# Kernel tuning notes

Measured on AMD Instinct MI355X. Metric: run time of the kernel, lower is better.

## Reference

```python
import jax, jax.numpy as jnp
import numpy as np

# --- fake-quant helpers (Brevitas-style simulated int4 with STE) ---

def _fq(x, scale, qmin, qmax):
    # fake quantize with straight-through estimator
    q = jnp.clip(jnp.round(x / scale), qmin, qmax) * scale
    return x + jax.lax.stop_gradient(q - x)

def quant_act_signed4(x):
    # signed 4-bit symmetric activation quant: scale = max|x| / 7
    scale = jax.lax.stop_gradient(jnp.maximum(jnp.max(jnp.abs(x)), 1e-8) / 7.0)
    return _fq(x, scale, -8, 7), scale

def quant_relu4(x):
    # QuantReLU: relu then unsigned 4-bit quant, scale = max / 15
    x = jax.nn.relu(x)
    scale = jax.lax.stop_gradient(jnp.maximum(jnp.max(x), 1e-8) / 15.0)
    return _fq(x, scale, 0, 15), scale

def quant_w4(w):
    # per-tensor symmetric 4-bit weight quant
    scale = jax.lax.stop_gradient(jnp.maximum(jnp.max(jnp.abs(w)), 1e-8) / 7.0)
    return _fq(w, scale, -8, 7), scale

def quant_bias32(b, in_scale, w_scale):
    # Int32Bias: bias quantized at scale = input_scale * weight_scale
    s = in_scale * w_scale
    return _fq(b, s, -(2.0**31), 2.0**31 - 1.0)

def conv2d(x, w, b):
    y = jax.lax.conv_general_dilated(x, w, (1, 1), 'VALID',
                                     dimension_numbers=('NCHW', 'OIHW', 'NCHW'))
    return y + b[None, :, None, None]


def setup_inputs() -> dict:
    key = jax.random.key(0)
    ks = jax.random.split(key, 9)
    f32 = jnp.float32
    return {
        'x':   jax.random.normal(ks[0], (32, 3, 224, 224), f32),
        'w1':  jax.random.normal(ks[1], (32, 3, 3, 3), f32) * 0.1,
        'b1':  jax.random.normal(ks[2], (32,), f32) * 0.05,
        'w2':  jax.random.normal(ks[3], (64, 32, 3, 3), f32) * 0.06,
        'b2':  jax.random.normal(ks[4], (64,), f32) * 0.05,
        'wf1': jax.random.normal(ks[5], (128, 64), f32) * 0.1,
        'bf1': jax.random.normal(ks[6], (128,), f32) * 0.05,
        'wf2': jax.random.normal(ks[7], (10, 128), f32) * 0.08,
        'bf2': jax.random.normal(ks[8], (10,), f32) * 0.05,
    }


def reference(x, w1, b1, w2, b2, wf1, bf1, wf2, bf2):
    # quant_inp
    xq, s_in = quant_act_signed4(x)
    # conv1 (quantized weights, Int32 bias)
    w1q, sw1 = quant_w4(w1)
    y = conv2d(xq, w1q, quant_bias32(b1, s_in, sw1))
    y, s1 = quant_relu4(y)
    # conv2
    w2q, sw2 = quant_w4(w2)
    y = conv2d(y, w2q, quant_bias32(b2, s1, sw2))
    y, s2 = quant_relu4(y)
    # adaptive avg pool to 1x1 + flatten -> [B, 64]
    y = jnp.mean(y, axis=(2, 3))
    # fc1
    wf1q, swf1 = quant_w4(wf1)
    y = y @ wf1q.T + quant_bias32(bf1, s2, swf1)
    y, s3 = quant_relu4(y)
    # fc2
    wf2q, swf2 = quant_w4(wf2)
    y = y @ wf2q.T + quant_bias32(bf2, s3, swf2)
    return jax.nn.log_softmax(y, axis=1)
```

## Files before the change

kernel.cpp:

```cpp
#include <hip/hip_runtime.h>
#include <cstdint>
#include <cstddef>

#define DI __device__ __forceinline__

typedef int v4i  __attribute__((ext_vector_type(4)));
typedef int v16i __attribute__((ext_vector_type(16)));

#if defined(__has_builtin)
#if __has_builtin(__builtin_amdgcn_sdot4)
#define HAS_SDOT4 1
#endif
#if __has_builtin(__builtin_amdgcn_alignbyte)
#define HAS_ALIGNBYTE 1
#endif
#if __has_builtin(__builtin_amdgcn_global_load_lds)
#define HAS_GLLDS 1
#endif
#if __has_builtin(__builtin_amdgcn_perm)
#define HAS_PERM 1
#endif
#endif

DI int dot4(unsigned a, unsigned b, int c) {
#ifdef HAS_SDOT4
  return __builtin_amdgcn_sdot4((int)a, (int)b, c, false);
#else
#pragma unroll
  for (int k = 0; k < 4; ++k)
    c += (int)(signed char)(a >> (8 * k)) * (int)(signed char)(b >> (8 * k));
  return c;
#endif
}

DI unsigned alignb(unsigned hi, unsigned lo, int sh) {
#ifdef HAS_ALIGNBYTE
  return __builtin_amdgcn_alignbyte(hi, lo, sh);
#else
  return sh ? ((lo >> (8 * sh)) | (hi << (32 - 8 * sh))) : lo;
#endif
}

DI unsigned bperm(unsigned hi, unsigned lo, unsigned sel) {
#ifdef HAS_PERM
  return __builtin_amdgcn_perm(hi, lo, sel);
#else
  unsigned r = 0;
#pragma unroll
  for (int i = 0; i < 4; ++i) {
    unsigned s = (sel >> (8 * i)) & 255u;
    unsigned b = (s < 4) ? (lo >> (8 * s)) : (hi >> (8 * (s - 4)));
    r |= (b & 255u) << (8 * i);
  }
  return r;
#endif
}

DI float qclamp(int a, float h) {
  return fminf(fmaxf(rintf((float)a * h), 0.f), 15.f);
}

DI unsigned pack4(float4 v, float s) {
  float f[4] = {v.x, v.y, v.z, v.w};
  unsigned w = 0;
#pragma unroll
  for (int k = 0; k < 4; ++k) {
    float q = rintf(f[k] / s);
    q = fminf(fmaxf(q, -8.f), 7.f);
    w |= ((unsigned)((int)q & 255)) << (8 * k);
  }
  return w;
}

#ifdef HAS_GLLDS
typedef __attribute__((address_space(1))) void glb_void;
typedef __attribute__((address_space(3))) void lds_void;
DI void gl_lds16(const void* g, void* l) {
  __builtin_amdgcn_global_load_lds((const glb_void*)g, (lds_void*)l, 16, 0, 0);
}
#else
DI void gl_lds16(const void* g, void* l) { *(v4i*)l = *(const v4i*)g; }
#endif

struct Scal {
  unsigned max_x, max_w1, max_w2, max_wf1, max_wf2;
  int max1, max2;
};

DI float mkscale(unsigned bits, float d) { return fmaxf(__uint_as_float(bits), 1e-8f) / d; }
DI float d_s_in(const Scal* sc) { return mkscale(sc->max_x, 7.f); }
DI float d_sw1(const Scal* sc)  { return mkscale(sc->max_w1, 7.f); }
DI float d_sw2(const Scal* sc)  { return mkscale(sc->max_w2, 7.f); }
DI float d_s1(const Scal* sc)   { return fmaxf((float)sc->max1 * (d_s_in(sc) * d_sw1(sc)), 1e-8f) / 15.f; }
DI float d_s2(const Scal* sc)   { return fmaxf((float)sc->max2 * (d_s1(sc) * d_sw2(sc)), 1e-8f) / 15.f; }

static constexpr int NX   = 32 * 3 * 224 * 224;
static constexpr int NP1  = 32 * 32 * 222 * 224;
static constexpr int C2_ROWB   = 224 * 32;
static constexpr int C2_HPLANE = 224 * 16;
static constexpr int C2_GRID = 32 * 110;

DI float wave_maxf(float v) { for (int o = 32; o; o >>= 1) v = fmaxf(v, __shfl_down(v, o, 64)); return v; }
DI int   wave_maxi(int v)   { for (int o = 32; o; o >>= 1) v = max(v, __shfl_down(v, o, 64));   return v; }

DI float block_maxf(float v) {
  __shared__ float s[8];
  v = wave_maxf(v);
  int lane = threadIdx.x & 63, w = threadIdx.x >> 6;
  int nw = (int)(blockDim.x >> 6);
  if (!lane) s[w] = v;
  __syncthreads();
  if (threadIdx.x < 64) {
    float t = ((int)threadIdx.x < nw) ? s[threadIdx.x] : 0.f;
    v = wave_maxf(t);
  }
  return v;
}

DI int block_maxi(int v) {
  __shared__ int s[8];
  v = wave_maxi(v);
  int lane = threadIdx.x & 63, w = threadIdx.x >> 6;
  int nw = (int)(blockDim.x >> 6);
  if (!lane) s[w] = v;
  __syncthreads();
  if (threadIdx.x < 64) {
    int t = ((int)threadIdx.x < nw) ? s[threadIdx.x] : 0;
    v = wave_maxi(t);
  }
  return v;
}

__global__ void k_absmax_xw(const float4* __restrict__ x, int n4,
                            const float* __restrict__ w1, const float* __restrict__ w2,
                            const float* __restrict__ wf1, const float* __restrict__ wf2,
                            Scal* sc) {
  if (blockIdx.x < 1024) {
    float m = 0.f;
    for (int i = blockIdx.x * 256 + threadIdx.x; i < n4; i += 1024 * 256) {
      float4 v = x[i];
      m = fmaxf(m, fmaxf(fmaxf(fabsf(v.x), fabsf(v.y)), fmaxf(fabsf(v.z), fabsf(v.w))));
    }
    m = block_maxf(m);
    if (!threadIdx.x) atomicMax(&sc->max_x, __float_as_uint(m));
    return;
  }
  const float* p; int n; unsigned* slot;
  int wb = blockIdx.x - 1024;
  if (wb == 0)      { p = w1;  n = 864;   slot = &sc->max_w1; }
  else if (wb == 1) { p = w2;  n = 18432; slot = &sc->max_w2; }
  else if (wb == 2) { p = wf1; n = 8192;  slot = &sc->max_wf1; }
  else              { p = wf2; n = 1280;  slot = &sc->max_wf2; }
  float m = 0.f;
  for (int i = threadIdx.x; i < n; i += 256) m = fmaxf(m, fabsf(p[i]));
  m = block_maxf(m);
  if (!threadIdx.x) atomicMax(slot, __float_as_uint(m));
}


DI void kpack0(const unsigned* R, v4i& f) {
  f[0] = (int)bperm(R[1], R[0], 0x04020100u);
  f[1] = (int)bperm(R[2], R[1], 0x05040201u);
  f[2] = (int)bperm(R[3], R[2], 0x06050402u);
  f[3] = (int)bperm(R[5], R[4], 0x04020100u);
}
DI void kpack1(const unsigned* R, v4i& f) {
  f[0] = (int)bperm(R[1], R[0], 0x05040201u);
  f[1] = (int)bperm(R[2], R[1], 0x06050402u);
  f[2] = (int)bperm(0u,   R[3], 0x04020100u);
  f[3] = 0;
}

DI v4i conv1_afrag(const unsigned* lw, int oc, int lhalf) {
  unsigned R[6];
  v4i f;
  if (lhalf == 0) {
#pragma unroll
    for (int s = 0; s < 6; ++s) R[s] = lw[oc * 9 + s];
    kpack0(R, f);
  } else {
#pragma unroll
    for (int s = 0; s < 4; ++s) R[s] = lw[oc * 9 + 5 + s];
    kpack1(R, f);
  }
  return f;
}

DI v4i conv1_bfrag(const signed char* lx, int oh_l, int qb, int sh, int lhalf) {
  unsigned R[6];
  v4i f;
  if (lhalf == 0) {
#pragma unroll
    for (int s = 0; s < 6; ++s) {
      int ic = s / 3, kh = s - ic * 3;
      const signed char* base = lx + (ic * 8 + oh_l + kh) * 224 + qb;
      unsigned d0 = *(const unsigned*)base;
      unsigned d1 = *(const unsigned*)(base + 4);
      R[s] = alignb(d1, d0, sh);
    }
    kpack0(R, f);
  } else {
#pragma unroll
    for (int s = 0; s < 4; ++s) {
      int seg = 5 + s;
      int ic = seg / 3, kh = seg - ic * 3;
      const signed char* base = lx + (ic * 8 + oh_l + kh) * 224 + qb;
      unsigned d0 = *(const unsigned*)base;
      unsigned d1 = *(const unsigned*)(base + 4);
      R[s] = alignb(d1, d0, sh);
    }
    kpack1(R, f);
  }
  return f;
}

DI void conv1_stage(const float4* x, const float* w1, const float* b1,
                    int b, int oh0, int tid, float s_in, float sw1,
                    signed char* lx, unsigned* lw, int* lb) {
  for (int i = tid; i < 288; i += 448) {
    int oc = i / 9, r = i - oc * 9;
    unsigned w = 0;
#pragma unroll
    for (int k = 0; k < 3; ++k) {
      float q = rintf(w1[oc * 27 + r * 3 + k] / sw1);
      q = fminf(fmaxf(q, -8.f), 7.f);
      w |= ((unsigned)((int)q & 255)) << (8 * k);
    }
    lw[i] = w;
  }
  if (tid < 32) lb[tid] = (int)rintf(b1[tid] / (s_in * sw1));
  const float4* src = x + (size_t)b * 3 * 224 * 56;
  unsigned* dst = (unsigned*)lx;
#pragma unroll
  for (int it = 0; it < 3; ++it) {
    int i = it * 448 + tid;
    int row = i / 56, d = i - row * 56;
    int ic = row >> 3, r = row & 7;
    dst[i] = pack4(src[(ic * 224 + (oh0 + r)) * 56 + d], s_in);
  }
}

__global__ void __launch_bounds__(448) k_conv1a(
    const float4* __restrict__ x, const float* __restrict__ w1,
    const float* __restrict__ b1, const float* __restrict__ w2,
    const Scal* __restrict__ sc, unsigned* __restrict__ w2frag,
    int* __restrict__ max1) {
  int tid = threadIdx.x;
  if (blockIdx.x >= 1184) {
    int j = (blockIdx.x - 1184) * 448 + tid;
    if (j < 4608) {
      int icq = j & 7; int t = j >> 3;
      int kw = t % 3; t /= 3;
      int kh = t % 3; int oc = t / 3;
      float s = d_sw2(sc);
      unsigned w = 0;
#pragma unroll
      for (int k = 0; k < 4; ++k) {
        int ic = icq * 4 + k;
        float q = rintf(w2[(oc * 32 + ic) * 9 + kh * 3 + kw] / s);
        q = fminf(fmaxf(q, -8.f), 7.f);
        w |= ((unsigned)((int)q & 255)) << (8 * k);
      }
      int tap = kh * 3 + kw;
      int dl = (oc & 31) | ((icq >> 2) << 5);
      w2frag[(((tap * 2) + (oc >> 5)) * 64 + dl) * 4 + (icq & 3)] = w;
    }
    return;
  }

  __shared__ signed char lx[3 * 8 * 224 + 16];
  __shared__ unsigned lw[288];
  __shared__ int lb[32];
  int strip = blockIdx.x % 37;
  int b = blockIdx.x / 37;
  int oh0 = strip * 6;
  float s_in = d_s_in(sc), sw1 = d_sw1(sc);
  conv1_stage(x, w1, b1, b, oh0, tid, s_in, sw1, lx, lw, lb);
  __syncthreads();

  int lane = tid & 63, wv = tid >> 6;
  int lane31 = lane & 31, lhalf = lane >> 5;
  int p = wv * 32 + lane31;
  int qb = p & ~3, sh = p & 3;
  v4i af = conv1_afrag(lw, lane31, lhalf);
  const v4i* lbv = (const v4i*)lb;
  v4i bq[4];
#pragma unroll
  for (int q = 0; q < 4; ++q) bq[q] = lbv[lhalf + 2 * q];

  int mx = 0;
#pragma unroll
  for (int oh_l = 0; oh_l < 6; ++oh_l) {
    v4i bf = conv1_bfrag(lx, oh_l, qb, sh, lhalf);
    v16i acc;
#pragma unroll
    for (int q = 0; q < 4; ++q)
#pragma unroll
      for (int j = 0; j < 4; ++j) acc[4 * q + j] = bq[q][j];
    acc = __builtin_amdgcn_mfma_i32_32x32x32_i8(af, bf, acc, 0, 0, 0);
    if (p < 222) {
#pragma unroll
      for (int r = 0; r < 16; ++r) mx = max(mx, acc[r]);
    }
  }
  mx = block_maxi(max(mx, 0));
  if (!tid) atomicMax(max1, mx);
}

__global__ void __launch_bounds__(448) k_conv1b(
    const float4* __restrict__ x, const float* __restrict__ w1,
    const float* __restrict__ b1, const Scal* __restrict__ sc,
    unsigned char* __restrict__ y1n) {
  __shared__ signed char lx[3 * 8 * 224 + 16];
  __shared__ unsigned lw[288];
  __shared__ int lb[32];
  int tid = threadIdx.x;
  int strip = blockIdx.x % 37;
  int b = blockIdx.x / 37;
  int oh0 = strip * 6;
  float s_in = d_s_in(sc), sw1 = d_sw1(sc);
  conv1_stage(x, w1, b1, b, oh0, tid, s_in, sw1, lx, lw, lb);
  __syncthreads();

  int lane = tid & 63, wv = tid >> 6;
  int lane31 = lane & 31, lhalf = lane >> 5;
  int p = wv * 32 + lane31;
  int qb = p & ~3, sh = p & 3;
  v4i af = conv1_afrag(lw, lane31, lhalf);
  const v4i* lbv = (const v4i*)lb;
  v4i bq[4];
#pragma unroll
  for (int q = 0; q < 4; ++q) bq[q] = lbv[lhalf + 2 * q];

  float h1 = (s_in * sw1) / d_s1(sc);

#pragma unroll
  for (int oh_l = 0; oh_l < 6; ++oh_l) {
    v4i bf = conv1_bfrag(lx, oh_l, qb, sh, lhalf);
    v16i acc;
#pragma unroll
    for (int q = 0; q < 4; ++q)
#pragma unroll
      for (int j = 0; j < 4; ++j) acc[4 * q + j] = bq[q][j];
    acc = __builtin_amdgcn_mfma_i32_32x32x32_i8(af, bf, acc, 0, 0, 0);
    if (p < 222) {
      size_t rowb = (size_t)(b * 222 + oh0 + oh_l) * C2_ROWB;
      unsigned char* dst0 = y1n + rowb + (size_t)p * 16;
#pragma unroll
      for (int q = 0; q < 4; ++q) {
        int oc0 = 8 * q + 4 * lhalf;
        unsigned cw = 0;
#pragma unroll
        for (int j = 0; j < 4; ++j)
          cw |= ((unsigned)(int)qclamp(acc[4 * q + j], h1)) << (8 * j);
        *(unsigned*)(dst0 + (oc0 >> 4) * C2_HPLANE + (oc0 & 15)) = cw;
      }
    }
  }
}


DI void c2_stage(const unsigned char* gA, const unsigned char* gW,
                 unsigned char* lA, unsigned* lw, int tid) {
  for (int c = tid; c < 2944; c += 448) {
    if (c < 1792) gl_lds16(gA + (size_t)c * 16, lA + c * 16);
    else          gl_lds16(gW + (size_t)(c - 1792) * 16,
                           (unsigned char*)lw + (size_t)(c - 1792) * 16);
  }
}

__global__ void __launch_bounds__(448, 4) k_conv2a(
    const unsigned char* __restrict__ y1n, const unsigned* __restrict__ w2frag,
    const float* __restrict__ b2, const Scal* __restrict__ sc, int* __restrict__ max2) {
  __shared__ __align__(16) unsigned char lA[4 * C2_ROWB];
  __shared__ __align__(16) unsigned lw[4608];
  __shared__ int lb2[64];
  int tid = threadIdx.x;
  int blk = (int)blockIdx.x;
  int logical = (blk & 7) * 440 + (blk >> 3);
  int b = logical / 110, ohg = logical - b * 110;
  int oh0 = ohg * 2;

  const unsigned char* gA = y1n + (size_t)(b * 222 + oh0) * C2_ROWB;
  c2_stage(gA, (const unsigned char*)w2frag, lA, lw, tid);
  if (tid < 64) {
    float sb = d_s1(sc) * d_sw2(sc);
    lb2[tid] = (int)rintf(b2[tid] / sb);
  }
  __syncthreads();

  int lane = tid & 63;
  int wv = tid >> 6;
  int lane31 = lane & 31, lhalf = lane >> 5;
  int ow0 = wv * 32;
  const unsigned char* Ab = lA + lhalf * C2_HPLANE + (size_t)(ow0 + lane31) * 16;
  int mx = 0;

  v4i a[4][3];
#pragma unroll
  for (int r = 0; r < 4; ++r)
#pragma unroll
    for (int kw = 0; kw < 3; ++kw)
      a[r][kw] = *(const v4i*)(Ab + (size_t)r * C2_ROWB + kw * 16);

#pragma unroll
  for (int h = 0; h < 2; ++h) {
    int bias = lb2[h * 32 + lane31];
    v16i acc0, acc1;
#pragma unroll
    for (int r = 0; r < 16; ++r) { acc0[r] = bias; acc1[r] = bias; }
#pragma unroll
    for (int kh = 0; kh < 3; ++kh)
#pragma unroll
      for (int kw = 0; kw < 3; ++kw) {
        int tap = kh * 3 + kw;
        v4i bb = *(const v4i*)(lw + (tap * 2 + h) * 256 + lane * 4);
        acc0 = __builtin_amdgcn_mfma_i32_32x32x32_i8(a[kh][kw], bb, acc0, 0, 0, 0);
        acc1 = __builtin_amdgcn_mfma_i32_32x32x32_i8(a[kh + 1][kw], bb, acc1, 0, 0, 0);
      }
    if (wv != 6) {
#pragma unroll
      for (int r = 0; r < 16; ++r) mx = max(mx, max(acc0[r], acc1[r]));
    } else {
#pragma unroll
      for (int r = 0; r < 16; ++r) {
        int m = (r & 3) + 8 * (r >> 2) + 4 * lhalf;
        if (ow0 + m < 220) mx = max(mx, max(acc0[r], acc1[r]));
      }
    }
  }
  mx = block_maxi(max(mx, 0));
  if (!tid) atomicMax(max2, mx);
}

__global__ void __launch_bounds__(448, 4) k_conv2b(
    const unsigned char* __restrict__ y1n, const unsigned* __restrict__ w2frag,
    const float* __restrict__ b2, const Scal* __restrict__ sc,
    int* __restrict__ pooled_i) {
  __shared__ __align__(16) unsigned char lA[4 * C2_ROWB];
  __shared__ __align__(16) unsigned lw[4608];
  __shared__ int lb2[64];
  __shared__ int ls[64];
  int tid = threadIdx.x;
  int blk = (int)blockIdx.x;
  int logical = (blk & 7) * 440 + (blk >> 3);
  int b = logical / 110, ohg = logical - b * 110;
  int oh0 = ohg * 2;

  const unsigned char* gA = y1n + (size_t)(b * 222 + oh0) * C2_ROWB;
  c2_stage(gA, (const unsigned char*)w2frag, lA, lw, tid);
  if (tid < 64) {
    float sb = d_s1(sc) * d_sw2(sc);
    lb2[tid] = (int)rintf(b2[tid] / sb);
    ls[tid] = 0;
  }
  __syncthreads();

  int lane = tid & 63;
  int wv = tid >> 6;
  int lane31 = lane & 31, lhalf = lane >> 5;
  int ow0 = wv * 32;
  const unsigned char* Ab = lA + lhalf * C2_HPLANE + (size_t)(ow0 + lane31) * 16;
  float h1 = (d_s1(sc) * d_sw2(sc)) * (1.0f / d_s2(sc));

  v4i a[4][3];
#pragma unroll
  for (int r = 0; r < 4; ++r)
#pragma unroll
    for (int kw = 0; kw < 3; ++kw)
      a[r][kw] = *(const v4i*)(Ab + (size_t)r * C2_ROWB + kw * 16);

#pragma unroll
  for (int h = 0; h < 2; ++h) {
    int bias = lb2[h * 32 + lane31];
    v16i acc0, acc1;
#pragma unroll
    for (int r = 0; r < 16; ++r) { acc0[r] = bias; acc1[r] = bias; }
#pragma unroll
    for (int kh = 0; kh < 3; ++kh)
#pragma unroll
      for (int kw = 0; kw < 3; ++kw) {
        int tap = kh * 3 + kw;
        v4i bb = *(const v4i*)(lw + (tap * 2 + h) * 256 + lane * 4);
        acc0 = __builtin_amdgcn_mfma_i32_32x32x32_i8(a[kh][kw], bb, acc0, 0, 0, 0);
        acc1 = __builtin_amdgcn_mfma_i32_32x32x32_i8(a[kh + 1][kw], bb, acc1, 0, 0, 0);
      }

    float fs = 0.f;
    if (wv != 6) {
#pragma unroll
      for (int r = 0; r < 16; ++r) fs += qclamp(acc0[r], h1) + qclamp(acc1[r], h1);
    } else {
#pragma unroll
      for (int r = 0; r < 16; ++r) {
        int m = (r & 3) + 8 * (r >> 2) + 4 * lhalf;
        if (ow0 + m < 220) fs += qclamp(acc0[r], h1) + qclamp(acc1[r], h1);
      }
    }
    int isum = (int)fs;
    isum += __shfl_down(isum, 32, 64);
    if (lhalf == 0) atomicAdd(&ls[h * 32 + lane31], isum);
  }
  __syncthreads();
  if (tid < 64) {
    int v = ls[tid];
    if (v != 0) atomicAdd(&pooled_i[b * 64 + tid], v);
  }
}

__global__ void __launch_bounds__(1024) k_fc(
    const int* __restrict__ pooled_i, const float* __restrict__ wf1,
    const float* __restrict__ bf1, const float* __restrict__ wf2,
    const float* __restrict__ bf2, const Scal* __restrict__ sc,
    float* __restrict__ out) {
  __shared__ float pl[2048];
  __shared__ float wq1[128 * 65];
  __shared__ float y3[32 * 130];
  __shared__ float zz[320];
  __shared__ float s3sh;
  __shared__ float red16[16];
  int tid = threadIdx.x;
  float swf1 = mkscale(sc->max_wf1, 7.f), swf2 = mkscale(sc->max_wf2, 7.f);
  float s2 = d_s2(sc);
  for (int i = tid; i < 2048; i += 1024) pl[i] = (float)pooled_i[i] * s2 / 48400.0f;
  for (int i = tid; i < 8192; i += 1024) {
    float q = rintf(wf1[i] / swf1);
    q = fminf(fmaxf(q, -8.f), 7.f);
    wq1[(i >> 6) * 65 + (i & 63)] = q * swf1;
  }
  __syncthreads();
  float sb1 = s2 * swf1;
  float lmax = 0.f;
#pragma unroll
  for (int o = tid; o < 4096; o += 1024) {
    int b = o >> 7, j = o & 127;
    float acc = rintf(bf1[j] / sb1) * sb1;
    const float* wrow = &wq1[j * 65];
    const float* xrow = &pl[b * 64];
#pragma unroll 16
    for (int k = 0; k < 64; ++k) acc += xrow[k] * wrow[k];
    float r = fmaxf(acc, 0.f);
    y3[b * 130 + j] = r;
    lmax = fmaxf(lmax, r);
  }
  lmax = wave_maxf(lmax);
  {
    int lane = tid & 63, w = tid >> 6;
    if (!lane) red16[w] = lmax;
  }
  __syncthreads();
  if (tid < 64) {
    float t = (tid < 16) ? red16[tid] : 0.f;
    t = wave_maxf(t);
    if (!tid) s3sh = fmaxf(t, 1e-8f) / 15.f;
  }
  __syncthreads();
  float s3 = s3sh;
  float sb2 = s3 * swf2;
  if (tid < 320) {
    int o = tid;
    int b = o / 10, j = o - b * 10;
    float acc = rintf(bf2[j] / sb2) * sb2;
    const float* yy = &y3[b * 130];
    const float* wrow = &wf2[j * 128];
#pragma unroll 16
    for (int k = 0; k < 128; ++k) {
      float q = rintf(yy[k] / s3);
      q = fminf(fmaxf(q, 0.f), 15.f);
      float wv = rintf(wrow[k] / swf2);
      wv = fminf(fmaxf(wv, -8.f), 7.f);
      acc += (q * s3) * (wv * swf2);
    }
    zz[o] = acc;
  }
  __syncthreads();
  if (tid < 32) {
    const float* z = &zz[tid * 10];
    float mm = z[0];
    for (int k = 1; k < 10; ++k) mm = fmaxf(mm, z[k]);
    float ssum = 0.f;
    for (int k = 0; k < 10; ++k) ssum += expf(z[k] - mm);
    float l = mm + logf(ssum);
    for (int k = 0; k < 10; ++k) out[tid * 10 + k] = z[k] - l;
  }
}

extern "C" void kernel_launch(void* const* d_in, const int* in_sizes, int n_in,
                              void* d_out, int out_size, void* d_ws, size_t ws_size,
                              hipStream_t stream) {
  const float* x   = (const float*)d_in[0];
  const float* w1  = (const float*)d_in[1];
  const float* b1  = (const float*)d_in[2];
  const float* w2  = (const float*)d_in[3];
  const float* b2  = (const float*)d_in[4];
  const float* wf1 = (const float*)d_in[5];
  const float* bf1 = (const float*)d_in[6];
  const float* wf2 = (const float*)d_in[7];
  const float* bf2 = (const float*)d_in[8];
  float* out = (float*)d_out;

  char* ws = (char*)d_ws;
  Scal* sc = (Scal*)ws;
  int* pooled_i = (int*)(ws + 1024);
  size_t off = 1024 + 8192;
  unsigned* w2frag = (unsigned*)(ws + off);     off += 4608 * 4;
  off = (off + 255) & ~(size_t)255;
  unsigned char* y1n = (unsigned char*)(ws + off); off += (size_t)NP1 + 256;
  (void)ws_size; (void)in_sizes; (void)n_in; (void)out_size;

  hipMemsetAsync(ws, 0, 1024 + 8192, stream);
  k_absmax_xw<<<1028, 256, 0, stream>>>((const float4*)x, NX / 4, w1, w2, wf1, wf2, sc);
  k_conv1a<<<1184 + 11, 448, 0, stream>>>((const float4*)x, w1, b1, w2, sc, w2frag, &sc->max1);
  k_conv1b<<<1184, 448, 0, stream>>>((const float4*)x, w1, b1, sc, y1n);
  k_conv2a<<<C2_GRID, 448, 0, stream>>>(y1n, w2frag, b2, sc, &sc->max2);
  k_conv2b<<<C2_GRID, 448, 0, stream>>>(y1n, w2frag, b2, sc, pooled_i);
  k_fc<<<1, 1024, 0, stream>>>(pooled_i, wf1, bf1, wf2, bf2, sc, out);
}
```

Baseline: 254.5 us.

## Process ten conv2 output rows per block with a rolling LDS row buffer

Each conv2 block now covers ten output rows instead of two. It walks them in five steps over a six-row LDS ring buffer and prefetches the next two input rows while computing the current ones. The aim is to cut redundant halo-row and weight staging traffic and the per-block setup, since the grid drops from 3520 to 704 blocks. In exchange, LDS per block grows, which may lower the number of blocks resident per CU, and the smaller grid can leave a tail-imbalanced final wave. A barrier is now added on every step.

```diff
diff --git a/kernel.cpp b/kernel.cpp
--- a/kernel.cpp
+++ b/kernel.cpp
@@ -98,7 +98,7 @@
 static constexpr int NP1  = 32 * 32 * 222 * 224;
 static constexpr int C2_ROWB   = 224 * 32;
 static constexpr int C2_HPLANE = 224 * 16;
-static constexpr int C2_GRID = 32 * 110;
+static constexpr int C2_BLOCKS = 704;
 
 DI float wave_maxf(float v) { for (int o = 32; o; o >>= 1) v = fmaxf(v, __shfl_down(v, o, 64)); return v; }
 DI int   wave_maxi(int v)   { for (int o = 32; o; o >>= 1) v = max(v, __shfl_down(v, o, 64));   return v; }
@@ -360,74 +360,82 @@
 }
 
 
-DI void c2_stage(const unsigned char* gA, const unsigned char* gW,
-                 unsigned char* lA, unsigned* lw, int tid) {
-  for (int c = tid; c < 2944; c += 448) {
-    if (c < 1792) gl_lds16(gA + (size_t)c * 16, lA + c * 16);
-    else          gl_lds16(gW + (size_t)(c - 1792) * 16,
-                           (unsigned char*)lw + (size_t)(c - 1792) * 16);
-  }
-}
-
 __global__ void __launch_bounds__(448, 4) k_conv2a(
     const unsigned char* __restrict__ y1n, const unsigned* __restrict__ w2frag,
     const float* __restrict__ b2, const Scal* __restrict__ sc, int* __restrict__ max2) {
-  __shared__ __align__(16) unsigned char lA[4 * C2_ROWB];
+  __shared__ __align__(16) unsigned char lA[6 * C2_ROWB];
   __shared__ __align__(16) unsigned lw[4608];
   __shared__ int lb2[64];
   int tid = threadIdx.x;
   int blk = (int)blockIdx.x;
-  int logical = (blk & 7) * 440 + (blk >> 3);
-  int b = logical / 110, ohg = logical - b * 110;
-  int oh0 = ohg * 2;
-
-  const unsigned char* gA = y1n + (size_t)(b * 222 + oh0) * C2_ROWB;
-  c2_stage(gA, (const unsigned char*)w2frag, lA, lw, tid);
+  int logical = (blk & 7) * 88 + (blk >> 3);
+  int b = logical / 22, j = logical - b * 22;
+  const unsigned char* gA = y1n + (size_t)(b * 222 + j * 10) * C2_ROWB;
+
+#pragma unroll
+  for (int r = 0; r < 4; ++r)
+    gl_lds16(gA + (size_t)r * C2_ROWB + (size_t)tid * 16,
+             lA + (size_t)r * C2_ROWB + (size_t)tid * 16);
+  {
+    const unsigned char* gW = (const unsigned char*)w2frag;
+    for (int c = tid; c < 1152; c += 448)
+      gl_lds16(gW + (size_t)c * 16, (unsigned char*)lw + (size_t)c * 16);
+  }
   if (tid < 64) {
     float sb = d_s1(sc) * d_sw2(sc);
     lb2[tid] = (int)rintf(b2[tid] / sb);
   }
   __syncthreads();
 
-  int lane = tid & 63;
-  int wv = tid >> 6;
+  int lane = tid & 63, wv = tid >> 6;
   int lane31 = lane & 31, lhalf = lane >> 5;
   int ow0 = wv * 32;
-  const unsigned char* Ab = lA + lhalf * C2_HPLANE + (size_t)(ow0 + lane31) * 16;
+  int pxoff = lhalf * C2_HPLANE + (ow0 + lane31) * 16;
   int mx = 0;
 
-  v4i a[4][3];
-#pragma unroll
-  for (int r = 0; r < 4; ++r)
-#pragma unroll
-    for (int kw = 0; kw < 3; ++kw)
-      a[r][kw] = *(const v4i*)(Ab + (size_t)r * C2_ROWB + kw * 16);
-
-#pragma unroll
-  for (int h = 0; h < 2; ++h) {
-    int bias = lb2[h * 32 + lane31];
-    v16i acc0, acc1;
-#pragma unroll
-    for (int r = 0; r < 16; ++r) { acc0[r] = bias; acc1[r] = bias; }
-#pragma unroll
-    for (int kh = 0; kh < 3; ++kh)
-#pragma unroll
-      for (int kw = 0; kw < 3; ++kw) {
-        int tap = kh * 3 + kw;
-        v4i bb = *(const v4i*)(lw + (tap * 2 + h) * 256 + lane * 4);
-        acc0 = __builtin_amdgcn_mfma_i32_32x32x32_i8(a[kh][kw], bb, acc0, 0, 0, 0);
-        acc1 = __builtin_amdgcn_mfma_i32_32x32x32_i8(a[kh + 1][kw], bb, acc1, 0, 0, 0);
+#pragma unroll
+  for (int i = 0; i < 5; ++i) {
+    if (i < 4) {
+      int ra = 4 + 2 * i;
+      gl_lds16(gA + (size_t)ra * C2_ROWB + (size_t)tid * 16,
+               lA + (size_t)(ra % 6) * C2_ROWB + (size_t)tid * 16);
+      gl_lds16(gA + (size_t)(ra + 1) * C2_ROWB + (size_t)tid * 16,
+               lA + (size_t)((ra + 1) % 6) * C2_ROWB + (size_t)tid * 16);
+    }
+    v4i a[4][3];
+#pragma unroll
+    for (int r = 0; r < 4; ++r)
+#pragma unroll
+      for (int kw = 0; kw < 3; ++kw)
+        a[r][kw] = *(const v4i*)(lA + (size_t)((2 * i + r) % 6) * C2_ROWB + pxoff + kw * 16);
+
+#pragma unroll
+    for (int h = 0; h < 2; ++h) {
+      int bias = lb2[h * 32 + lane31];
+      v16i acc0, acc1;
+#pragma unroll
+      for (int r = 0; r < 16; ++r) { acc0[r] = bias; acc1[r] = bias; }
+#pragma unroll
+      for (int kh = 0; kh < 3; ++kh)
+#pragma unroll
+        for (int kw = 0; kw < 3; ++kw) {
+          int tap = kh * 3 + kw;
+          v4i bb = *(const v4i*)(lw + (tap * 2 + h) * 256 + lane * 4);
+          acc0 = __builtin_amdgcn_mfma_i32_32x32x32_i8(a[kh][kw], bb, acc0, 0, 0, 0);
+          acc1 = __builtin_amdgcn_mfma_i32_32x32x32_i8(a[kh + 1][kw], bb, acc1, 0, 0, 0);
+        }
+      if (wv != 6) {
+#pragma unroll
+        for (int r = 0; r < 16; ++r) mx = max(mx, max(acc0[r], acc1[r]));
+      } else {
+#pragma unroll
+        for (int r = 0; r < 16; ++r) {
+          int m = (r & 3) + 8 * (r >> 2) + 4 * lhalf;
+          if (ow0 + m < 220) mx = max(mx, max(acc0[r], acc1[r]));
+        }
       }
-    if (wv != 6) {
-#pragma unroll
-      for (int r = 0; r < 16; ++r) mx = max(mx, max(acc0[r], acc1[r]));
-    } else {
-#pragma unroll
-      for (int r = 0; r < 16; ++r) {
-        int m = (r & 3) + 8 * (r >> 2) + 4 * lhalf;
-        if (ow0 + m < 220) mx = max(mx, max(acc0[r], acc1[r]));
-      }
-    }
+    }
+    __syncthreads();
   }
   mx = block_maxi(max(mx, 0));
   if (!tid) atomicMax(max2, mx);
@@ -437,18 +445,25 @@
     const unsigned char* __restrict__ y1n, const unsigned* __restrict__ w2frag,
     const float* __restrict__ b2, const Scal* __restrict__ sc,
     int* __restrict__ pooled_i) {
-  __shared__ __align__(16) unsigned char lA[4 * C2_ROWB];
+  __shared__ __align__(16) unsigned char lA[6 * C2_ROWB];
   __shared__ __align__(16) unsigned lw[4608];
   __shared__ int lb2[64];
   __shared__ int ls[64];
   int tid = threadIdx.x;
   int blk = (int)blockIdx.x;
-  int logical = (blk & 7) * 440 + (blk >> 3);
-  int b = logical / 110, ohg = logical - b * 110;
-  int oh0 = ohg * 2;
-
-  const unsigned char* gA = y1n + (size_t)(b * 222 + oh0) * C2_ROWB;
-  c2_stage(gA, (const unsigned char*)w2frag, lA, lw, tid);
+  int logical = (blk & 7) * 88 + (blk >> 3);
+  int b = logical / 22, j = logical - b * 22;
+  const unsigned char* gA = y1n + (size_t)(b * 222 + j * 10) * C2_ROWB;
+
+#pragma unroll
+  for (int r = 0; r < 4; ++r)
+    gl_lds16(gA + (size_t)r * C2_ROWB + (size_t)tid * 16,
+             lA + (size_t)r * C2_ROWB + (size_t)tid * 16);
+  {
+    const unsigned char* gW = (const unsigned char*)w2frag;
+    for (int c = tid; c < 1152; c += 448)
+      gl_lds16(gW + (size_t)c * 16, (unsigned char*)lw + (size_t)c * 16);
+  }
   if (tid < 64) {
     float sb = d_s1(sc) * d_sw2(sc);
     lb2[tid] = (int)rintf(b2[tid] / sb);
@@ -456,52 +471,61 @@
   }
   __syncthreads();
 
-  int lane = tid & 63;
-  int wv = tid >> 6;
+  int lane = tid & 63, wv = tid >> 6;
   int lane31 = lane & 31, lhalf = lane >> 5;
   int ow0 = wv * 32;
-  const unsigned char* Ab = lA + lhalf * C2_HPLANE + (size_t)(ow0 + lane31) * 16;
+  int pxoff = lhalf * C2_HPLANE + (ow0 + lane31) * 16;
   float h1 = (d_s1(sc) * d_sw2(sc)) * (1.0f / d_s2(sc));
 
-  v4i a[4][3];
-#pragma unroll
-  for (int r = 0; r < 4; ++r)
-#pragma unroll
-    for (int kw = 0; kw < 3; ++kw)
-      a[r][kw] = *(const v4i*)(Ab + (size_t)r * C2_ROWB + kw * 16);
-
-#pragma unroll
-  for (int h = 0; h < 2; ++h) {
-    int bias = lb2[h * 32 + lane31];
-    v16i acc0, acc1;
-#pragma unroll
-    for (int r = 0; r < 16; ++r) { acc0[r] = bias; acc1[r] = bias; }
-#pragma unroll
-    for (int kh = 0; kh < 3; ++kh)
-#pragma unroll
-      for (int kw = 0; kw < 3; ++kw) {
-        int tap = kh * 3 + kw;
-        v4i bb = *(const v4i*)(lw + (tap * 2 + h) * 256 + lane * 4);
-        acc0 = __builtin_amdgcn_mfma_i32_32x32x32_i8(a[kh][kw], bb, acc0, 0, 0, 0);
-        acc1 = __builtin_amdgcn_mfma_i32_32x32x32_i8(a[kh + 1][kw], bb, acc1, 0, 0, 0);
+#pragma unroll
+  for (int i = 0; i < 5; ++i) {
+    if (i < 4) {
+      int ra = 4 + 2 * i;
+      gl_lds16(gA + (size_t)ra * C2_ROWB + (size_t)tid * 16,
+               lA + (size_t)(ra % 6) * C2_ROWB + (size_t)tid * 16);
+      gl_lds16(gA + (size_t)(ra + 1) * C2_ROWB + (size_t)tid * 16,
+               lA + (size_t)((ra + 1) % 6) * C2_ROWB + (size_t)tid * 16);
+    }
+    v4i a[4][3];
+#pragma unroll
+    for (int r = 0; r < 4; ++r)
+#pragma unroll
+      for (int kw = 0; kw < 3; ++kw)
+        a[r][kw] = *(const v4i*)(lA + (size_t)((2 * i + r) % 6) * C2_ROWB + pxoff + kw * 16);
+
+#pragma unroll
+    for (int h = 0; h < 2; ++h) {
+      int bias = lb2[h * 32 + lane31];
+      v16i acc0, acc1;
+#pragma unroll
+      for (int r = 0; r < 16; ++r) { acc0[r] = bias; acc1[r] = bias; }
+#pragma unroll
+      for (int kh = 0; kh < 3; ++kh)
+#pragma unroll
+        for (int kw = 0; kw < 3; ++kw) {
+          int tap = kh * 3 + kw;
+          v4i bb = *(const v4i*)(lw + (tap * 2 + h) * 256 + lane * 4);
+          acc0 = __builtin_amdgcn_mfma_i32_32x32x32_i8(a[kh][kw], bb, acc0, 0, 0, 0);
+          acc1 = __builtin_amdgcn_mfma_i32_32x32x32_i8(a[kh + 1][kw], bb, acc1, 0, 0, 0);
+        }
+
+      float fs = 0.f;
+      if (wv != 6) {
+#pragma unroll
+        for (int r = 0; r < 16; ++r) fs += qclamp(acc0[r], h1) + qclamp(acc1[r], h1);
+      } else {
+#pragma unroll
+        for (int r = 0; r < 16; ++r) {
+          int m = (r & 3) + 8 * (r >> 2) + 4 * lhalf;
+          if (ow0 + m < 220) fs += qclamp(acc0[r], h1) + qclamp(acc1[r], h1);
+        }
       }
-
-    float fs = 0.f;
-    if (wv != 6) {
-#pragma unroll
-      for (int r = 0; r < 16; ++r) fs += qclamp(acc0[r], h1) + qclamp(acc1[r], h1);
-    } else {
-#pragma unroll
-      for (int r = 0; r < 16; ++r) {
-        int m = (r & 3) + 8 * (r >> 2) + 4 * lhalf;
-        if (ow0 + m < 220) fs += qclamp(acc0[r], h1) + qclamp(acc1[r], h1);
-      }
-    }
-    int isum = (int)fs;
-    isum += __shfl_down(isum, 32, 64);
-    if (lhalf == 0) atomicAdd(&ls[h * 32 + lane31], isum);
-  }
-  __syncthreads();
+      int isum = (int)fs;
+      isum += __shfl_down(isum, 32, 64);
+      if (lhalf == 0) atomicAdd(&ls[h * 32 + lane31], isum);
+    }
+    __syncthreads();
+  }
   if (tid < 64) {
     int v = ls[tid];
     if (v != 0) atomicAdd(&pooled_i[b * 64 + tid], v);
@@ -612,7 +636,7 @@
   k_absmax_xw<<<1028, 256, 0, stream>>>((const float4*)x, NX / 4, w1, w2, wf1, wf2, sc);
   k_conv1a<<<1184 + 11, 448, 0, stream>>>((const float4*)x, w1, b1, w2, sc, w2frag, &sc->max1);
   k_conv1b<<<1184, 448, 0, stream>>>((const float4*)x, w1, b1, sc, y1n);
-  k_conv2a<<<C2_GRID, 448, 0, stream>>>(y1n, w2frag, b2, sc, &sc->max2);
-  k_conv2b<<<C2_GRID, 448, 0, stream>>>(y1n, w2frag, b2, sc, pooled_i);
+  k_conv2a<<<C2_BLOCKS, 448, 0, stream>>>(y1n, w2frag, b2, sc, &sc->max2);
+  k_conv2b<<<C2_BLOCKS, 448, 0, stream>>>(y1n, w2frag, b2, sc, pooled_i);
   k_fc<<<1, 1024, 0, stream>>>(pooled_i, wf1, bf1, wf2, bf2, sc, out);
 }
```

After: 236.5 us. -7.1%, faster.

## Make conv2 kernels persistent per-wave tile loops with direct global A loads

Applied to the files above, without the earlier changes.

Both conv2 kernels now launch 1232 blocks of 256 threads. Each wave loops over 5 (batch, row-pair, column-group) tiles instead of one block handling a full row pair with 7 waves. The activation tile is no longer staged through LDS but read directly from global memory into registers, and weights and bias are staged once per block. This spreads the LDS weight staging and launch cost across more work per block and drops the activation LDS footprint to raise occupancy. The cost is uncoalesced-ish direct global loads and a two-slot pooled accumulator to handle tiles that cross a batch boundary.

```diff
diff --git a/kernel.cpp b/kernel.cpp
--- a/kernel.cpp
+++ b/kernel.cpp
@@ -98,7 +98,8 @@
 static constexpr int NP1  = 32 * 32 * 222 * 224;
 static constexpr int C2_ROWB   = 224 * 32;
 static constexpr int C2_HPLANE = 224 * 16;
-static constexpr int C2_GRID = 32 * 110;
+static constexpr int C2_BLK    = 1232;
+static constexpr int C2_TPW    = 5;
 
 DI float wave_maxf(float v) { for (int o = 32; o; o >>= 1) v = fmaxf(v, __shfl_down(v, o, 64)); return v; }
 DI int   wave_maxi(int v)   { for (int o = 32; o; o >>= 1) v = max(v, __shfl_down(v, o, 64));   return v; }
@@ -360,72 +361,74 @@
 }
 
 
-DI void c2_stage(const unsigned char* gA, const unsigned char* gW,
-                 unsigned char* lA, unsigned* lw, int tid) {
-  for (int c = tid; c < 2944; c += 448) {
-    if (c < 1792) gl_lds16(gA + (size_t)c * 16, lA + c * 16);
-    else          gl_lds16(gW + (size_t)(c - 1792) * 16,
-                           (unsigned char*)lw + (size_t)(c - 1792) * 16);
-  }
-}
-
-__global__ void __launch_bounds__(448, 4) k_conv2a(
+DI void c2w_stage(const unsigned* w2frag, unsigned* lw, const float* b2,
+                  const Scal* sc, int* lb2, int tid) {
+  const unsigned char* gW = (const unsigned char*)w2frag;
+  for (int c = tid; c < 1152; c += 256)
+    gl_lds16(gW + (size_t)c * 16, (unsigned char*)lw + (size_t)c * 16);
+  if (tid < 64) {
+    float sb = d_s1(sc) * d_sw2(sc);
+    lb2[tid] = (int)rintf(b2[tid] / sb);
+  }
+}
+
+__global__ void __launch_bounds__(256, 4) k_conv2a(
     const unsigned char* __restrict__ y1n, const unsigned* __restrict__ w2frag,
     const float* __restrict__ b2, const Scal* __restrict__ sc, int* __restrict__ max2) {
-  __shared__ __align__(16) unsigned char lA[4 * C2_ROWB];
   __shared__ __align__(16) unsigned lw[4608];
   __shared__ int lb2[64];
   int tid = threadIdx.x;
+  c2w_stage(w2frag, lw, b2, sc, lb2, tid);
+  __syncthreads();
+
+  int lane = tid & 63, wv = tid >> 6;
+  int lane31 = lane & 31, lhalf = lane >> 5;
   int blk = (int)blockIdx.x;
-  int logical = (blk & 7) * 440 + (blk >> 3);
-  int b = logical / 110, ohg = logical - b * 110;
-  int oh0 = ohg * 2;
-
-  const unsigned char* gA = y1n + (size_t)(b * 222 + oh0) * C2_ROWB;
-  c2_stage(gA, (const unsigned char*)w2frag, lA, lw, tid);
-  if (tid < 64) {
-    float sb = d_s1(sc) * d_sw2(sc);
-    lb2[tid] = (int)rintf(b2[tid] / sb);
-  }
-  __syncthreads();
-
-  int lane = tid & 63;
-  int wv = tid >> 6;
-  int lane31 = lane & 31, lhalf = lane >> 5;
-  int ow0 = wv * 32;
-  const unsigned char* Ab = lA + lhalf * C2_HPLANE + (size_t)(ow0 + lane31) * 16;
+  int blk2 = (blk & 7) * 154 + (blk >> 3);
+  int t0 = (blk2 * 4 + wv) * C2_TPW;
+  int bias0 = lb2[lane31], bias1 = lb2[32 + lane31];
+  int aoff = lhalf * C2_HPLANE + lane31 * 16;
   int mx = 0;
 
-  v4i a[4][3];
-#pragma unroll
-  for (int r = 0; r < 4; ++r)
-#pragma unroll
-    for (int kw = 0; kw < 3; ++kw)
-      a[r][kw] = *(const v4i*)(Ab + (size_t)r * C2_ROWB + kw * 16);
-
-#pragma unroll
-  for (int h = 0; h < 2; ++h) {
-    int bias = lb2[h * 32 + lane31];
-    v16i acc0, acc1;
-#pragma unroll
-    for (int r = 0; r < 16; ++r) { acc0[r] = bias; acc1[r] = bias; }
-#pragma unroll
-    for (int kh = 0; kh < 3; ++kh)
-#pragma unroll
-      for (int kw = 0; kw < 3; ++kw) {
-        int tap = kh * 3 + kw;
-        v4i bb = *(const v4i*)(lw + (tap * 2 + h) * 256 + lane * 4);
-        acc0 = __builtin_amdgcn_mfma_i32_32x32x32_i8(a[kh][kw], bb, acc0, 0, 0, 0);
-        acc1 = __builtin_amdgcn_mfma_i32_32x32x32_i8(a[kh + 1][kw], bb, acc1, 0, 0, 0);
-      }
-    if (wv != 6) {
-#pragma unroll
-      for (int r = 0; r < 16; ++r) mx = max(mx, max(acc0[r], acc1[r]));
-    } else {
-#pragma unroll
-      for (int r = 0; r < 16; ++r) {
-        int m = (r & 3) + 8 * (r >> 2) + 4 * lhalf;
-        if (ow0 + m < 220) mx = max(mx, max(acc0[r], acc1[r]));
+#pragma unroll 1
+  for (int u = 0; u < C2_TPW; ++u) {
+    int t = t0 + u;
+    int owg = t % 7; int tt = t / 7;
+    int pair = tt % 110; int b = tt / 110;
+    int oh0 = pair * 2, ow0 = owg * 32;
+    const unsigned char* Ab = y1n + (size_t)(b * 222 + oh0) * C2_ROWB
+                              + (size_t)(aoff + ow0 * 16);
+    v4i a[4][3];
+#pragma unroll
+    for (int r = 0; r < 4; ++r)
+#pragma unroll
+      for (int kw = 0; kw < 3; ++kw)
+        a[r][kw] = *(const v4i*)(Ab + (size_t)r * C2_ROWB + kw * 16);
+
+#pragma unroll
+    for (int h = 0; h < 2; ++h) {
+      int bias = (h == 0) ? bias0 : bias1;
+      v16i acc0, acc1;
+#pragma unroll
+      for (int r = 0; r < 16; ++r) { acc0[r] = bias; acc1[r] = bias; }
+#pragma unroll
+      for (int kh = 0; kh < 3; ++kh)
+#pragma unroll
+        for (int kw = 0; kw < 3; ++kw) {
+          int tap = kh * 3 + kw;
+          v4i bb = *(const v4i*)(lw + (tap * 2 + h) * 256 + lane * 4);
+          acc0 = __builtin_amdgcn_mfma_i32_32x32x32_i8(a[kh][kw], bb, acc0, 0, 0, 0);
+          acc1 = __builtin_amdgcn_mfma_i32_32x32x32_i8(a[kh + 1][kw], bb, acc1, 0, 0, 0);
+        }
+      if (owg != 6) {
+#pragma unroll
+        for (int r = 0; r < 16; ++r) mx = max(mx, max(acc0[r], acc1[r]));
+      } else {
+#pragma unroll
+        for (int r = 0; r < 16; ++r) {
+          int m = (r & 3) + 8 * (r >> 2) + 4 * lhalf;
+          if (ow0 + m < 220) mx = max(mx, max(acc0[r], acc1[r]));
+        }
       }
     }
   }
@@ -433,78 +436,81 @@
   if (!tid) atomicMax(max2, mx);
 }
 
-__global__ void __launch_bounds__(448, 4) k_conv2b(
+__global__ void __launch_bounds__(256, 4) k_conv2b(
     const unsigned char* __restrict__ y1n, const unsigned* __restrict__ w2frag,
     const float* __restrict__ b2, const Scal* __restrict__ sc,
     int* __restrict__ pooled_i) {
-  __shared__ __align__(16) unsigned char lA[4 * C2_ROWB];
   __shared__ __align__(16) unsigned lw[4608];
   __shared__ int lb2[64];
-  __shared__ int ls[64];
+  __shared__ int ls[128];
   int tid = threadIdx.x;
+  c2w_stage(w2frag, lw, b2, sc, lb2, tid);
+  if (tid < 128) ls[tid] = 0;
+  __syncthreads();
+
+  int lane = tid & 63, wv = tid >> 6;
+  int lane31 = lane & 31, lhalf = lane >> 5;
   int blk = (int)blockIdx.x;
-  int logical = (blk & 7) * 440 + (blk >> 3);
-  int b = logical / 110, ohg = logical - b * 110;
-  int oh0 = ohg * 2;
-
-  const unsigned char* gA = y1n + (size_t)(b * 222 + oh0) * C2_ROWB;
-  c2_stage(gA, (const unsigned char*)w2frag, lA, lw, tid);
-  if (tid < 64) {
-    float sb = d_s1(sc) * d_sw2(sc);
-    lb2[tid] = (int)rintf(b2[tid] / sb);
-    ls[tid] = 0;
-  }
-  __syncthreads();
-
-  int lane = tid & 63;
-  int wv = tid >> 6;
-  int lane31 = lane & 31, lhalf = lane >> 5;
-  int ow0 = wv * 32;
-  const unsigned char* Ab = lA + lhalf * C2_HPLANE + (size_t)(ow0 + lane31) * 16;
+  int blk2 = (blk & 7) * 154 + (blk >> 3);
+  int t0 = (blk2 * 4 + wv) * C2_TPW;
+  int b_first = (blk2 * 4 * C2_TPW) / 770;
+  int bias0 = lb2[lane31], bias1 = lb2[32 + lane31];
+  int aoff = lhalf * C2_HPLANE + lane31 * 16;
   float h1 = (d_s1(sc) * d_sw2(sc)) * (1.0f / d_s2(sc));
 
-  v4i a[4][3];
-#pragma unroll
-  for (int r = 0; r < 4; ++r)
-#pragma unroll
-    for (int kw = 0; kw < 3; ++kw)
-      a[r][kw] = *(const v4i*)(Ab + (size_t)r * C2_ROWB + kw * 16);
-
-#pragma unroll
-  for (int h = 0; h < 2; ++h) {
-    int bias = lb2[h * 32 + lane31];
-    v16i acc0, acc1;
-#pragma unroll
-    for (int r = 0; r < 16; ++r) { acc0[r] = bias; acc1[r] = bias; }
-#pragma unroll
-    for (int kh = 0; kh < 3; ++kh)
-#pragma unroll
-      for (int kw = 0; kw < 3; ++kw) {
-        int tap = kh * 3 + kw;
-        v4i bb = *(const v4i*)(lw + (tap * 2 + h) * 256 + lane * 4);
-        acc0 = __builtin_amdgcn_mfma_i32_32x32x32_i8(a[kh][kw], bb, acc0, 0, 0, 0);
-        acc1 = __builtin_amdgcn_mfma_i32_32x32x32_i8(a[kh + 1][kw], bb, acc1, 0, 0, 0);
+#pragma unroll 1
+  for (int u = 0; u < C2_TPW; ++u) {
+    int t = t0 + u;
+    int owg = t % 7; int tt = t / 7;
+    int pair = tt % 110; int b = tt / 110;
+    int oh0 = pair * 2, ow0 = owg * 32;
+    int slot = b - b_first;
+    const unsigned char* Ab = y1n + (size_t)(b * 222 + oh0) * C2_ROWB
+                              + (size_t)(aoff + ow0 * 16);
+    v4i a[4][3];
+#pragma unroll
+    for (int r = 0; r < 4; ++r)
+#pragma unroll
+      for (int kw = 0; kw < 3; ++kw)
+        a[r][kw] = *(const v4i*)(Ab + (size_t)r * C2_ROWB + kw * 16);
+
+#pragma unroll
+    for (int h = 0; h < 2; ++h) {
+      int bias = (h == 0) ? bias0 : bias1;
+      v16i acc0, acc1;
+#pragma unroll
+      for (int r = 0; r < 16; ++r) { acc0[r] = bias; acc1[r] = bias; }
+#pragma unroll
+      for (int kh = 0; kh < 3; ++kh)
+#pragma unroll
+        for (int kw = 0; kw < 3; ++kw) {
+          int tap = kh * 3 + kw;
+          v4i bb = *(const v4i*)(lw + (tap * 2 + h) * 256 + lane * 4);
+          acc0 = __builtin_amdgcn_mfma_i32_32x32x32_i8(a[kh][kw], bb, acc0, 0, 0, 0);
+          acc1 = __builtin_amdgcn_mfma_i32_32x32x32_i8(a[kh + 1][kw], bb, acc1, 0, 0, 0);
+        }
+
+      float fs = 0.f;
+      if (owg != 6) {
+#pragma unroll
+        for (int r = 0; r < 16; ++r) fs += qclamp(acc0[r], h1) + qclamp(acc1[r], h1);
+      } else {
+#pragma unroll
+        for (int r = 0; r < 16; ++r) {
+          int m = (r & 3) + 8 * (r >> 2) + 4 * lhalf;
+          if (ow0 + m < 220) fs += qclamp(acc0[r], h1) + qclamp(acc1[r], h1);
+        }
       }
-
-    float fs = 0.f;
-    if (wv != 6) {
-#pragma unroll
-      for (int r = 0; r < 16; ++r) fs += qclamp(acc0[r], h1) + qclamp(acc1[r], h1);
-    } else {
-#pragma unroll
-      for (int r = 0; r < 16; ++r) {
-        int m = (r & 3) + 8 * (r >> 2) + 4 * lhalf;
-        if (ow0 + m < 220) fs += qclamp(acc0[r], h1) + qclamp(acc1[r], h1);
-      }
-    }
-    int isum = (int)fs;
-    isum += __shfl_down(isum, 32, 64);
-    if (lhalf == 0) atomicAdd(&ls[h * 32 + lane31], isum);
-  }
-  __syncthreads();
-  if (tid < 64) {
+      int isum = (int)fs;
+      isum += __shfl_down(isum, 32, 64);
+      if (lhalf == 0) atomicAdd(&ls[slot * 64 + h * 32 + lane31], isum);
+    }
+  }
+  __syncthreads();
+  if (tid < 128) {
+    int bb = b_first + (tid >> 6);
     int v = ls[tid];
-    if (v != 0) atomicAdd(&pooled_i[b * 64 + tid], v);
+    if (bb < 32 && v != 0) atomicAdd(&pooled_i[bb * 64 + (tid & 63)], v);
   }
 }
 
@@ -612,7 +618,7 @@
   k_absmax_xw<<<1028, 256, 0, stream>>>((const float4*)x, NX / 4, w1, w2, wf1, wf2, sc);
   k_conv1a<<<1184 + 11, 448, 0, stream>>>((const float4*)x, w1, b1, w2, sc, w2frag, &sc->max1);
   k_conv1b<<<1184, 448, 0, stream>>>((const float4*)x, w1, b1, sc, y1n);
-  k_conv2a<<<C2_GRID, 448, 0, stream>>>(y1n, w2frag, b2, sc, &sc->max2);
-  k_conv2b<<<C2_GRID, 448, 0, stream>>>(y1n, w2frag, b2, sc, pooled_i);
+  k_conv2a<<<C2_BLK, 256, 0, stream>>>(y1n, w2frag, b2, sc, &sc->max2);
+  k_conv2b<<<C2_BLK, 256, 0, stream>>>(y1n, w2frag, b2, sc, pooled_i);
   k_fc<<<1, 1024, 0, stream>>>(pooled_i, wf1, bf1, wf2, bf2, sc, out);
 }
```

New measurement: 374.7 us. +47.2%, slower.
